# Optimization experiments

Hardware: AMD Instinct MI355X
Metric: run time of the kernel (lower is better)

Reference implementation:

```python
import jax, jax.numpy as jnp
import numpy as np

H = 51  # n_hidden
B = 8192  # batch
T = 2048  # seq_len
FUTURE = 64


def setup_inputs() -> dict:
    key = jax.random.key(0)
    ks = jax.random.split(key, 12)
    s = 1.0 / np.sqrt(H)
    u = lambda k, shape: jax.random.uniform(k, shape, jnp.float32, -s, s)
    return {
        "x": jax.random.normal(ks[0], (B, T), jnp.float32),
        "W_ih1": u(ks[1], (4 * H, 1)),
        "W_hh1": u(ks[2], (4 * H, H)),
        "b_ih1": u(ks[3], (4 * H,)),
        "b_hh1": u(ks[4], (4 * H,)),
        "W_ih2": u(ks[5], (4 * H, H)),
        "W_hh2": u(ks[6], (4 * H, H)),
        "b_ih2": u(ks[7], (4 * H,)),
        "b_hh2": u(ks[8], (4 * H,)),
        "W_out": u(ks[9], (1, H)),
        "b_out": u(ks[10], (1,)),
        "future": FUTURE,
    }


def _lstm_cell(x, h, c, Wih, Whh, bih, bhh):
    # PyTorch LSTMCell: gates ordered i, f, g, o
    g = x @ Wih.T + h @ Whh.T + (bih + bhh)  # [B, 4H]
    i, f, gg, o = jnp.split(g, 4, axis=-1)
    i = jax.nn.sigmoid(i)
    f = jax.nn.sigmoid(f)
    gg = jnp.tanh(gg)
    o = jax.nn.sigmoid(o)
    c2 = f * c + i * gg
    h2 = o * jnp.tanh(c2)
    return h2, c2


def reference(x, W_ih1, W_hh1, b_ih1, b_hh1, W_ih2, W_hh2, b_ih2, b_hh2,
              W_out, b_out, future):
    Bn = x.shape[0]
    h1 = jnp.zeros((Bn, H), x.dtype)
    c1 = jnp.zeros((Bn, H), x.dtype)

    def emit(h1, c1):
        # Quirk of the original code: layer-2 state is layer-1's CURRENT (h1, c1),
        # and layer-2's own state is never carried forward.
        h2, _ = _lstm_cell(h1, h1, c1, W_ih2, W_hh2, b_ih2, b_hh2)
        return h2 @ W_out.T + b_out  # [B, 1]

    def step(carry, xt):
        h1, c1 = carry
        h1, c1 = _lstm_cell(xt, h1, c1, W_ih1, W_hh1, b_ih1, b_hh1)
        out = emit(h1, c1)
        return (h1, c1), out

    xs = jnp.swapaxes(x, 0, 1)[:, :, None]  # [T, B, 1]
    (h1, c1), outs = jax.lax.scan(step, (h1, c1), xs)
    outs = outs[..., 0].T  # [B, T]

    def fstep(carry, _):
        h1, c1, out = carry
        h1, c1 = _lstm_cell(out, h1, c1, W_ih1, W_hh1, b_ih1, b_hh1)
        out = emit(h1, c1)
        return (h1, c1, out), out

    last = outs[:, -1:]
    _, fouts = jax.lax.scan(fstep, (h1, c1, last), None, length=future)
    fouts = fouts[..., 0].T if future > 0 else jnp.zeros((Bn, 0), x.dtype)
    return jnp.concatenate([outs, fouts], axis=1)  # [B, T + future]
```

## Files before the change

### kernel.cpp

```cpp
#include <hip/hip_runtime.h>

#define HH   51
#define H4   204
#define TSEQ 2048
#define FUT  64
#define TT   (TSEQ + FUT)
#define RPB  16
#define NTH  1024
#define HSTR 80

typedef _Float16 h8 __attribute__((ext_vector_type(8)));
typedef float    f4 __attribute__((ext_vector_type(4)));

#define LOG2E 1.44269504f

__device__ __forceinline__ float sigm_f(float z) {
    return __builtin_amdgcn_rcpf(1.0f + __builtin_amdgcn_exp2f(-LOG2E * z));
}
__device__ __forceinline__ float tanh_f(float z) {
    return __builtin_fmaf(2.0f,
        __builtin_amdgcn_rcpf(1.0f + __builtin_amdgcn_exp2f(-2.0f * LOG2E * z)), -1.0f);
}

__global__ __launch_bounds__(NTH, 8)
void lstm_kernel(const float* __restrict__ x,
                 const float* __restrict__ Wih1, const float* __restrict__ Whh1,
                 const float* __restrict__ bih1, const float* __restrict__ bhh1,
                 const float* __restrict__ Wih2, const float* __restrict__ Whh2,
                 const float* __restrict__ bih2, const float* __restrict__ bhh2,
                 const float* __restrict__ Wout, const float* __restrict__ bout,
                 float* __restrict__ out)
{
    __shared__ _Float16 hbuf[2][RPB][HSTR];
    __shared__ float part[2][13][17];
    __shared__ float wouts[64];

    const int tid  = threadIdx.x;
    const int lane = tid & 63;
    const int w    = tid >> 6;
    const int quad = lane >> 4;
    const int nl   = lane & 15;
    const int rb   = blockIdx.x * RPB;

    if (tid < 64) wouts[tid] = (tid < HH) ? Wout[tid] : 0.0f;
    for (int i = tid; i < 2 * RPB * HSTR; i += NTH) (&hbuf[0][0][0])[i] = (_Float16)0.0f;
    __syncthreads();
    if (tid < RPB) {
        hbuf[0][tid][0]  = (_Float16)x[(size_t)(rb + tid) * TSEQ];
        hbuf[0][tid][52] = (_Float16)1.0f;  hbuf[0][tid][53] = (_Float16)1.0f;
        hbuf[1][tid][52] = (_Float16)1.0f;  hbuf[1][tid][53] = (_Float16)1.0f;
    }
    const float bo = bout[0];

    h8 W1[2], W2[2];
    if (w < 13) {
        const int jp = 16 * w + nl;
        const int kk = jp >> 2, q = jp & 3;
        const bool valid = (jp < H4);
        const int jrow = q * HH + kk;
        float b1 = 0.0f, b2 = 0.0f;
        if (valid) { b1 = bih1[jrow] + bhh1[jrow]; b2 = bih2[jrow] + bhh2[jrow]; }
        const _Float16 b1h = (_Float16)b1, b2h = (_Float16)b2;
        const _Float16 b1l = (_Float16)(b1 - (float)b1h), b2l = (_Float16)(b2 - (float)b2h);
        #pragma unroll
        for (int s = 0; s < 2; ++s) {
            h8 w1v, w2v;
            #pragma unroll
            for (int j = 0; j < 8; ++j) {
                const int k = s * 32 + quad * 8 + j;
                _Float16 a1 = (_Float16)0.0f, a2 = (_Float16)0.0f;
                if (valid) {
                    if (k == 0) {
                        a1 = (_Float16)Wih1[jrow];
                    } else if (k <= HH) {
                        const int o = jrow * HH + (k - 1);
                        a1 = (_Float16)Whh1[o];
                        a2 = (_Float16)(Wih2[o] + Whh2[o]);
                    } else if (k == 52) { a1 = b1h; a2 = b2h; }
                    else if (k == 53)   { a1 = b1l; a2 = b2l; }
                }
                w1v[j] = a1;
                w2v[j] = a2;
            }
            W1[s] = w1v;
            W2[s] = w2v;
        }
    }

    float xnext = 0.0f;
    if (w == 14 && lane < RPB) xnext = x[(size_t)(rb + lane) * TSEQ + 1];

    const int kh = 4 * w + quad;
    float c1 = 0.0f;
    __syncthreads();

    for (int t = 0; t < TT; ++t) {
        const int cur = t & 1, nxt = cur ^ 1;

        if (w < 13) {
            const h8 Bh0 = *(const h8*)&hbuf[cur][nl][quad * 8];
            const h8 Bh1 = *(const h8*)&hbuf[cur][nl][32 + quad * 8];
            f4 g = {0.f, 0.f, 0.f, 0.f};
            g = __builtin_amdgcn_mfma_f32_16x16x32_f16(W1[0], Bh0, g, 0, 0, 0);
            g = __builtin_amdgcn_mfma_f32_16x16x32_f16(W1[1], Bh1, g, 0, 0, 0);
            const float ig = sigm_f(g[0]);
            const float fg = sigm_f(g[1]);
            const float gg = tanh_f(g[2]);
            const float og = sigm_f(g[3]);
            c1 = fg * c1 + ig * gg;
            const float h1v = og * tanh_f(c1);
            if (kh < HH) hbuf[nxt][nl][1 + kh] = (_Float16)h1v;
        } else if (w == 13) {
            if (t >= 1 && t <= TSEQ - 1 && lane < RPB) {
                float s = bo;
                #pragma unroll
                for (int j = 0; j < 13; ++j) s += part[cur ^ 1][j][lane];
                out[(size_t)(rb + lane) * TT + (t - 1)] = s;
            }
        } else if (w == 14) {
            if (lane < RPB) {
                if (t + 1 < TSEQ) hbuf[nxt][lane][0] = (_Float16)xnext;
                if (t + 2 < TSEQ) xnext = x[(size_t)(rb + lane) * TSEQ + (t + 2)];
            }
        }
        __syncthreads();

        if (w < 13) {
            const h8 Bh0 = *(const h8*)&hbuf[nxt][nl][quad * 8];
            const h8 Bh1 = *(const h8*)&hbuf[nxt][nl][32 + quad * 8];
            f4 g = {0.f, 0.f, 0.f, 0.f};
            g = __builtin_amdgcn_mfma_f32_16x16x32_f16(W2[0], Bh0, g, 0, 0, 0);
            g = __builtin_amdgcn_mfma_f32_16x16x32_f16(W2[1], Bh1, g, 0, 0, 0);
            const float ig = sigm_f(g[0]);
            const float fg = sigm_f(g[1]);
            const float gg = tanh_f(g[2]);
            const float og = sigm_f(g[3]);
            const float c2 = fg * c1 + ig * gg;
            float p = og * tanh_f(c2) * wouts[kh];
            p += __shfl_xor(p, 16, 64);
            p += __shfl_xor(p, 32, 64);
            if (quad == 0) part[cur][w][nl] = p;
        }
        __syncthreads();

        if (t >= TSEQ - 1) {
            if (w == 13 && lane < RPB) {
                float s = bo;
                #pragma unroll
                for (int j = 0; j < 13; ++j) s += part[cur][j][lane];
                out[(size_t)(rb + lane) * TT + t] = s;
                hbuf[nxt][lane][0] = (_Float16)s;
            }
            __syncthreads();
        }
    }
}

extern "C" void kernel_launch(void* const* d_in, const int* in_sizes, int n_in,
                              void* d_out, int out_size, void* d_ws, size_t ws_size,
                              hipStream_t stream) {
    (void)in_sizes; (void)n_in; (void)d_ws; (void)ws_size; (void)out_size;
    const float* x    = (const float*)d_in[0];
    const float* Wih1 = (const float*)d_in[1];
    const float* Whh1 = (const float*)d_in[2];
    const float* bih1 = (const float*)d_in[3];
    const float* bhh1 = (const float*)d_in[4];
    const float* Wih2 = (const float*)d_in[5];
    const float* Whh2 = (const float*)d_in[6];
    const float* bih2 = (const float*)d_in[7];
    const float* bhh2 = (const float*)d_in[8];
    const float* Wout = (const float*)d_in[9];
    const float* bout = (const float*)d_in[10];
    float* outp = (float*)d_out;

    dim3 grid(8192 / RPB);
    dim3 block(NTH);
    hipLaunchKernelGGL(lstm_kernel, grid, block, 0, stream,
                       x, Wih1, Whh1, bih1, bhh1, Wih2, Whh2, bih2, bhh2,
                       Wout, bout, outp);
}
```

Baseline: 2.957 ms.

## Skew layer-2 emission by one step to halve barriers in teacher-forced loop

During the teacher-forced phase, the layer-2 emit for step t-1 is now computed from the same h buffer read for layer-1 step t. Both MFMA pairs share one set of operand loads, which cuts the per-step barrier count from two to one. An epilogue emits the last teacher-forced output, and the autoregressive phase keeps its original three-barrier structure. The x-prefetch and output-reduce wave roles are merged into one wave, dropping the block from 1024 to 896 threads, and the LDS row stride shrinks.

After: 3.491 ms. 18.1% more time.

```diff
diff --git a/kernel.cpp b/kernel.cpp
--- a/kernel.cpp
+++ b/kernel.cpp
@@ -6,8 +6,8 @@
 #define FUT  64
 #define TT   (TSEQ + FUT)
 #define RPB  16
-#define NTH  1024
-#define HSTR 80
+#define NTH  896
+#define HSTR 72
 
 typedef _Float16 h8 __attribute__((ext_vector_type(8)));
 typedef float    f4 __attribute__((ext_vector_type(4)));
@@ -22,7 +22,7 @@
         __builtin_amdgcn_rcpf(1.0f + __builtin_amdgcn_exp2f(-2.0f * LOG2E * z)), -1.0f);
 }
 
-__global__ __launch_bounds__(NTH, 8)
+__global__ __launch_bounds__(NTH, 7)
 void lstm_kernel(const float* __restrict__ x,
                  const float* __restrict__ Wih1, const float* __restrict__ Whh1,
                  const float* __restrict__ bih1, const float* __restrict__ bhh1,
@@ -87,72 +87,136 @@
         }
     }
 
+    const int kh = 4 * w + quad;
+    const size_t obase = (size_t)(rb + (lane & 15)) * TT;
+    const size_t xbase = (size_t)(rb + (lane & 15)) * TSEQ;
     float xnext = 0.0f;
-    if (w == 14 && lane < RPB) xnext = x[(size_t)(rb + lane) * TSEQ + 1];
-
-    const int kh = 4 * w + quad;
+    if (w == 13 && lane < RPB) xnext = x[xbase + 1];
     float c1 = 0.0f;
     __syncthreads();
-
-    for (int t = 0; t < TT; ++t) {
+    const float wk = (w < 13) ? wouts[kh] : 0.0f;
+
+    for (int t = 0; t < TSEQ; ++t) {
         const int cur = t & 1, nxt = cur ^ 1;
-
         if (w < 13) {
-            const h8 Bh0 = *(const h8*)&hbuf[cur][nl][quad * 8];
-            const h8 Bh1 = *(const h8*)&hbuf[cur][nl][32 + quad * 8];
-            f4 g = {0.f, 0.f, 0.f, 0.f};
-            g = __builtin_amdgcn_mfma_f32_16x16x32_f16(W1[0], Bh0, g, 0, 0, 0);
-            g = __builtin_amdgcn_mfma_f32_16x16x32_f16(W1[1], Bh1, g, 0, 0, 0);
-            const float ig = sigm_f(g[0]);
-            const float fg = sigm_f(g[1]);
-            const float gg = tanh_f(g[2]);
-            const float og = sigm_f(g[3]);
+            const _Float16* hb = &hbuf[cur][nl][0];
+            const h8 Bh0 = *(const h8*)(hb + quad * 8);
+            const h8 Bh1 = *(const h8*)(hb + 32 + quad * 8);
+            f4 g1 = {0.f, 0.f, 0.f, 0.f}, g2 = {0.f, 0.f, 0.f, 0.f};
+            g1 = __builtin_amdgcn_mfma_f32_16x16x32_f16(W1[0], Bh0, g1, 0, 0, 0);
+            g1 = __builtin_amdgcn_mfma_f32_16x16x32_f16(W1[1], Bh1, g1, 0, 0, 0);
+            g2 = __builtin_amdgcn_mfma_f32_16x16x32_f16(W2[0], Bh0, g2, 0, 0, 0);
+            g2 = __builtin_amdgcn_mfma_f32_16x16x32_f16(W2[1], Bh1, g2, 0, 0, 0);
+            const float c_prev = c1;
+            {
+                const float ig = sigm_f(g1[0]);
+                const float fg = sigm_f(g1[1]);
+                const float gg = tanh_f(g1[2]);
+                const float og = sigm_f(g1[3]);
+                c1 = fg * c1 + ig * gg;
+                const float h1v = og * tanh_f(c1);
+                if (kh < HH) hbuf[nxt][nl][1 + kh] = (_Float16)h1v;
+            }
+            {
+                const float ig = sigm_f(g2[0]);
+                const float fg = sigm_f(g2[1]);
+                const float gg = tanh_f(g2[2]);
+                const float og = sigm_f(g2[3]);
+                const float c2 = fg * c_prev + ig * gg;
+                float p = og * tanh_f(c2) * wk;
+                p += __shfl_xor(p, 16, 64);
+                p += __shfl_xor(p, 32, 64);
+                if (quad == 0) part[cur][w][nl] = p;
+            }
+        } else if (lane < RPB) {
+            if (t >= 2) {
+                float s = bo;
+                #pragma unroll
+                for (int j = 0; j < 13; ++j) s += part[nxt][j][lane];
+                out[obase + (t - 2)] = s;
+            }
+            if (t + 1 < TSEQ) hbuf[nxt][lane][0] = (_Float16)xnext;
+            if (t + 2 < TSEQ) xnext = x[xbase + (t + 2)];
+        }
+        __syncthreads();
+    }
+
+    if (w < 13) {
+        const _Float16* hb = &hbuf[0][nl][0];
+        const h8 Bh0 = *(const h8*)(hb + quad * 8);
+        const h8 Bh1 = *(const h8*)(hb + 32 + quad * 8);
+        f4 g2 = {0.f, 0.f, 0.f, 0.f};
+        g2 = __builtin_amdgcn_mfma_f32_16x16x32_f16(W2[0], Bh0, g2, 0, 0, 0);
+        g2 = __builtin_amdgcn_mfma_f32_16x16x32_f16(W2[1], Bh1, g2, 0, 0, 0);
+        const float ig = sigm_f(g2[0]);
+        const float fg = sigm_f(g2[1]);
+        const float gg = tanh_f(g2[2]);
+        const float og = sigm_f(g2[3]);
+        const float c2 = fg * c1 + ig * gg;
+        float p = og * tanh_f(c2) * wk;
+        p += __shfl_xor(p, 16, 64);
+        p += __shfl_xor(p, 32, 64);
+        if (quad == 0) part[0][w][nl] = p;
+    } else if (lane < RPB) {
+        float s = bo;
+        #pragma unroll
+        for (int j = 0; j < 13; ++j) s += part[1][j][lane];
+        out[obase + (TSEQ - 2)] = s;
+    }
+    __syncthreads();
+    if (w == 13 && lane < RPB) {
+        float s = bo;
+        #pragma unroll
+        for (int j = 0; j < 13; ++j) s += part[0][j][lane];
+        out[obase + (TSEQ - 1)] = s;
+        hbuf[0][lane][0] = (_Float16)s;
+    }
+    __syncthreads();
+
+    for (int t = TSEQ; t < TT; ++t) {
+        const int cur = t & 1, nxt = cur ^ 1;
+        if (w < 13) {
+            const _Float16* hb = &hbuf[cur][nl][0];
+            const h8 Bh0 = *(const h8*)(hb + quad * 8);
+            const h8 Bh1 = *(const h8*)(hb + 32 + quad * 8);
+            f4 g1 = {0.f, 0.f, 0.f, 0.f};
+            g1 = __builtin_amdgcn_mfma_f32_16x16x32_f16(W1[0], Bh0, g1, 0, 0, 0);
+            g1 = __builtin_amdgcn_mfma_f32_16x16x32_f16(W1[1], Bh1, g1, 0, 0, 0);
+            const float ig = sigm_f(g1[0]);
+            const float fg = sigm_f(g1[1]);
+            const float gg = tanh_f(g1[2]);
+            const float og = sigm_f(g1[3]);
             c1 = fg * c1 + ig * gg;
             const float h1v = og * tanh_f(c1);
             if (kh < HH) hbuf[nxt][nl][1 + kh] = (_Float16)h1v;
-        } else if (w == 13) {
-            if (t >= 1 && t <= TSEQ - 1 && lane < RPB) {
-                float s = bo;
-                #pragma unroll
-                for (int j = 0; j < 13; ++j) s += part[cur ^ 1][j][lane];
-                out[(size_t)(rb + lane) * TT + (t - 1)] = s;
-            }
-        } else if (w == 14) {
-            if (lane < RPB) {
-                if (t + 1 < TSEQ) hbuf[nxt][lane][0] = (_Float16)xnext;
-                if (t + 2 < TSEQ) xnext = x[(size_t)(rb + lane) * TSEQ + (t + 2)];
-            }
-        }
-        __syncthreads();
-
+        }
+        __syncthreads();
         if (w < 13) {
-            const h8 Bh0 = *(const h8*)&hbuf[nxt][nl][quad * 8];
-            const h8 Bh1 = *(const h8*)&hbuf[nxt][nl][32 + quad * 8];
-            f4 g = {0.f, 0.f, 0.f, 0.f};
-            g = __builtin_amdgcn_mfma_f32_16x16x32_f16(W2[0], Bh0, g, 0, 0, 0);
-            g = __builtin_amdgcn_mfma_f32_16x16x32_f16(W2[1], Bh1, g, 0, 0, 0);
-            const float ig = sigm_f(g[0]);
-            const float fg = sigm_f(g[1]);
-            const float gg = tanh_f(g[2]);
-            const float og = sigm_f(g[3]);
+            const _Float16* hb = &hbuf[nxt][nl][0];
+            const h8 Bh0 = *(const h8*)(hb + quad * 8);
+            const h8 Bh1 = *(const h8*)(hb + 32 + quad * 8);
+            f4 g2 = {0.f, 0.f, 0.f, 0.f};
+            g2 = __builtin_amdgcn_mfma_f32_16x16x32_f16(W2[0], Bh0, g2, 0, 0, 0);
+            g2 = __builtin_amdgcn_mfma_f32_16x16x32_f16(W2[1], Bh1, g2, 0, 0, 0);
+            const float ig = sigm_f(g2[0]);
+            const float fg = sigm_f(g2[1]);
+            const float gg = tanh_f(g2[2]);
+            const float og = sigm_f(g2[3]);
             const float c2 = fg * c1 + ig * gg;
-            float p = og * tanh_f(c2) * wouts[kh];
+            float p = og * tanh_f(c2) * wk;
             p += __shfl_xor(p, 16, 64);
             p += __shfl_xor(p, 32, 64);
             if (quad == 0) part[cur][w][nl] = p;
         }
         __syncthreads();
-
-        if (t >= TSEQ - 1) {
-            if (w == 13 && lane < RPB) {
-                float s = bo;
-                #pragma unroll
-                for (int j = 0; j < 13; ++j) s += part[cur][j][lane];
-                out[(size_t)(rb + lane) * TT + t] = s;
-                hbuf[nxt][lane][0] = (_Float16)s;
-            }
-            __syncthreads();
-        }
+        if (w == 13 && lane < RPB) {
+            float s = bo;
+            #pragma unroll
+            for (int j = 0; j < 13; ++j) s += part[cur][j][lane];
+            out[obase + t] = s;
+            if (t + 1 < TT) hbuf[nxt][lane][0] = (_Float16)s;
+        }
+        __syncthreads();
     }
 }
 
```
